# Kernel optimization log

Measured on AMD Instinct MI355X. Metric: run time of the kernel, lower is better.

## Reference

```python
import jax, jax.numpy as jnp
import numpy as np
from jax.ops import segment_sum

N0 = 50000
N1 = 50000
E = 300000
D = 128
L = 3
EPS_GIN = 0.1
COEF = 0.1
BN_EPS = 1e-5


def setup_inputs() -> dict:
    key = jax.random.key(0)
    ks = jax.random.split(key, 32)
    inp = {}
    inp['x0'] = jax.random.randint(ks[0], (N0, 2), 0, 3)
    inp['x1'] = jax.random.randint(ks[1], (N1, 2), 0, 3)
    inp['ei101'] = jax.random.randint(ks[2], (2, E), 0, N1)
    inp['ea101'] = jax.random.randint(ks[3], (E, 2), 0, 3)
    inp['ei110'] = jax.random.randint(ks[4], (2, E), 0, N0)  # src '1' -> dst '0' (N1==N0)
    inp['ea110'] = jax.random.randint(ks[5], (E, 2), 0, 3)
    inp['ei021'] = jax.random.randint(ks[6], (2, E), 0, N1)  # src '0' -> dst '1'
    inp['ea021'] = jax.random.randint(ks[7], (E, 2), 0, 3)
    inp['ei030'] = jax.random.randint(ks[8], (2, E), 0, N0)
    inp['ea030'] = jax.random.randint(ks[9], (E, 2), 0, 3)
    # learned parameters
    s = 0.05
    inp['x_emb1'] = jax.random.normal(ks[10], (120, D), jnp.float32) * s
    inp['x_emb2'] = jax.random.normal(ks[11], (3, D), jnp.float32) * s
    inp['e_emb1'] = jax.random.normal(ks[12], (6, D), jnp.float32) * s
    inp['e_emb2'] = jax.random.normal(ks[13], (3, D), jnp.float32) * s
    w = 1.0 / np.sqrt(D)
    inp['gin_w1'] = jax.random.normal(ks[14], (D, 2 * D), jnp.float32) * w
    inp['gin_b1'] = jnp.zeros((2 * D,), jnp.float32)
    inp['gin_w2'] = jax.random.normal(ks[15], (2 * D, D), jnp.float32) * (1.0 / np.sqrt(2 * D))
    inp['gin_b2'] = jnp.zeros((D,), jnp.float32)
    inp['w110'] = jax.random.normal(ks[16], (D, D), jnp.float32) * w
    inp['b110'] = jnp.zeros((D,), jnp.float32)
    inp['w021'] = jax.random.normal(ks[17], (D, D), jnp.float32) * w
    inp['b021'] = jnp.zeros((D,), jnp.float32)
    inp['w030'] = jax.random.normal(ks[18], (D, D), jnp.float32) * w
    inp['b030'] = jnp.zeros((D,), jnp.float32)
    inp['bn_gamma'] = jnp.ones((L, D), jnp.float32)
    inp['bn_beta'] = jnp.zeros((L, D), jnp.float32)
    return inp


def _add_self_loops(ei, ea, n):
    loop = jnp.arange(n, dtype=ei.dtype)
    ei = jnp.concatenate([ei, jnp.stack([loop, loop])], axis=1)
    self_attr = jnp.tile(jnp.array([[4, 0]], dtype=ea.dtype), (n, 1))
    return ei, jnp.concatenate([ea, self_attr], axis=0)


def _bn(x, gamma, beta):
    # training-mode BatchNorm1d: batch statistics, biased variance
    mu = jnp.mean(x, axis=0)
    var = jnp.var(x, axis=0)
    return (x - mu) * jax.lax.rsqrt(var + BN_EPS) * gamma + beta


def reference(x0, x1, ei101, ea101, ei110, ea110, ei021, ea021, ei030, ea030,
              x_emb1, x_emb2, e_emb1, e_emb2,
              gin_w1, gin_b1, gin_w2, gin_b2,
              w110, b110, w021, b021, w030, b030,
              bn_gamma, bn_beta):
    n0, n1 = x0.shape[0], x1.shape[0]
    # AddSelfLoops only for homogeneous edge types, fill_value=[4,0]
    ei101, ea101 = _add_self_loops(ei101, ea101, n1)
    ei030, ea030 = _add_self_loops(ei030, ea030, n0)

    h0 = x_emb1[x0[:, 0]] + x_emb2[x0[:, 1]]
    h1 = x_emb1[x1[:, 0]] + x_emb2[x1[:, 1]]
    e101 = e_emb1[ea101[:, 0]] + e_emb2[ea101[:, 1]]
    e110 = e_emb1[ea110[:, 0]] + e_emb2[ea110[:, 1]]
    e021 = e_emb1[ea021[:, 0]] + e_emb2[ea021[:, 1]]
    e030 = e_emb1[ea030[:, 0]] + e_emb2[ea030[:, 1]]

    def gin(h_src, h_dst, ei, eattr):
        agg = segment_sum(h_src[ei[0]] + eattr, ei[1], num_segments=h_dst.shape[0])
        z = agg + (1.0 + EPS_GIN) * h_dst
        return jnp.maximum(z @ gin_w1 + gin_b1, 0.0) @ gin_w2 + gin_b2

    def lin(h_src, n_dst, ei, eattr, w, b):
        agg = segment_sum(h_src[ei[0]] + eattr, ei[1], num_segments=n_dst)
        return (agg @ w + b) * COEF

    for layer in range(L):
        # HeteroConv aggr='mean' over convs sharing a destination node type
        out1 = 0.5 * (gin(h1, h1, ei101, e101) + lin(h0, n1, ei021, e021, w021, b021))
        out0 = 0.5 * (lin(h1, n0, ei110, e110, w110, b110) + lin(h0, n0, ei030, e030, w030, b030))
        g, b = bn_gamma[layer], bn_beta[layer]
        h0, h1 = _bn(out0, g, b), _bn(out1, g, b)
        if layer < L - 1:
            h0, h1 = jax.nn.relu(h0), jax.nn.relu(h1)
    # to_homogeneous().x: node types in order '0', '1'
    return jnp.concatenate([h0, h1], axis=0)
```

## Files before the change

### kernel.cpp

```cpp
#include <hip/hip_runtime.h>

#define D 128
#define BN_EPS 1e-5f
#define MAXNB 16

typedef __attribute__((ext_vector_type(8))) short bf16x8;
typedef __attribute__((ext_vector_type(4))) float f32x4;

__device__ __forceinline__ unsigned short f2bf(float x) {
  unsigned u = __float_as_uint(x);
  u += 0x7FFF + ((u >> 16) & 1);
  return (unsigned short)(u >> 16);
}

__device__ __forceinline__ void cvt8(float (&f)[8], bf16x8 r) {
  const unsigned* u = (const unsigned*)&r;
#pragma unroll
  for (int j = 0; j < 4; ++j) {
    f[2 * j] = __uint_as_float(u[j] << 16);
    f[2 * j + 1] = __uint_as_float(u[j] & 0xFFFF0000u);
  }
}

__global__ __launch_bounds__(256) void k_etbl(const float* __restrict__ e1,
                                              const float* __restrict__ e2,
                                              float* __restrict__ etbl) {
  int idx = blockIdx.x * 256 + threadIdx.x;
  if (idx < 9 * D) {
    int combo = idx / D, c = idx % D;
    etbl[idx] = e1[(combo / 3) * D + c] + e2[(combo % 3) * D + c];
  } else if (idx < 10 * D) {
    int c = idx - 9 * D;
    etbl[idx] = e1[4 * D + c] + e2[c];
  }
}

__global__ __launch_bounds__(256) void k_embed(const int* __restrict__ x,
                                               const float* __restrict__ emb1,
                                               const float* __restrict__ emb2,
                                               unsigned short* __restrict__ out,
                                               int n) {
  int idx = blockIdx.x * 256 + threadIdx.x;
  if (idx >= n * 32) return;
  int node = idx >> 5, c4 = idx & 31;
  int i1 = x[2 * node], i2 = x[2 * node + 1];
  float4 v1 = *(const float4*)(emb1 + (size_t)i1 * D + c4 * 4);
  float4 v2 = *(const float4*)(emb2 + (size_t)i2 * D + c4 * 4);
  ushort4 o;
  o.x = f2bf(v1.x + v2.x); o.y = f2bf(v1.y + v2.y);
  o.z = f2bf(v1.z + v2.z); o.w = f2bf(v1.w + v2.w);
  *(ushort4*)(out + (size_t)node * D + c4 * 4) = o;
}

__global__ __launch_bounds__(256) void k_wprep(const float* __restrict__ W,
                                               unsigned short* __restrict__ Wt,
                                               int K, int N, float scale) {
  int idx = blockIdx.x * 256 + threadIdx.x;
  if (idx >= K * N) return;
  int n = idx / K, k = idx - n * K;
  Wt[idx] = f2bf(W[(size_t)k * N + n] * scale);
}

__global__ __launch_bounds__(256) void k_bprep(
    const float* __restrict__ b110, const float* __restrict__ b030,
    const float* __restrict__ gb1, const float* __restrict__ gb2,
    const float* __restrict__ b021, float* __restrict__ bias0,
    float* __restrict__ biash, float* __restrict__ bias1) {
  int i = threadIdx.x;
  if (i < 128) {
    bias0[i] = 0.05f * (b110[i] + b030[i]);
    bias1[i] = 0.5f * gb2[i] + 0.05f * b021[i];
  }
  biash[i] = gb1[i];
}

struct EdgeArr {
  const int* ei[4];
  const int* ea[4];
  int* cur[4];
  int* pay[4];
};
struct CsrPtrs {
  int* cur[4];
  int* rp[4];
  int n[4];
};

__global__ __launch_bounds__(256) void k_hist4(EdgeArr A, int E) {
  int t = blockIdx.y;
  int e = blockIdx.x * 256 + threadIdx.x;
  if (e >= E) return;
  atomicAdd(&A.cur[t][A.ei[t][E + e]], 1);
}

__global__ __launch_bounds__(256) void k_scan1(CsrPtrs p, int* __restrict__ bsum) {
  __shared__ int lds[256];
  int type = blockIdx.y;
  const int* cur = p.cur[type];
  int n = p.n[type];
  int base = blockIdx.x * 4096;
  int s = 0;
  for (int i = threadIdx.x; i < 4096; i += 256) {
    int idx = base + i;
    if (idx < n) s += cur[idx];
  }
  int tid = threadIdx.x;
  lds[tid] = s;
  __syncthreads();
  for (int off = 128; off > 0; off >>= 1) {
    if (tid < off) lds[tid] += lds[tid + off];
    __syncthreads();
  }
  if (tid == 0) bsum[type * MAXNB + blockIdx.x] = lds[0];
}

__global__ __launch_bounds__(64) void k_scan2(int* __restrict__ bsum) {
  int t = threadIdx.x;
  if (t < 4) {
    int run = 0;
    for (int i = 0; i < MAXNB; ++i) {
      int v = bsum[t * MAXNB + i];
      bsum[t * MAXNB + i] = run;
      run += v;
    }
  }
}

__global__ __launch_bounds__(256) void k_scan3(CsrPtrs p,
                                               const int* __restrict__ bsum,
                                               int E) {
  __shared__ int lds[256];
  int type = blockIdx.y;
  int* cur = p.cur[type];
  int* rp = p.rp[type];
  int n = p.n[type];
  int tid = threadIdx.x;
  if (blockIdx.x == 0 && tid == 0) rp[n] = E;
  int t0 = blockIdx.x * 4096 + tid * 16;
  int loc[16];
  int s = 0;
#pragma unroll
  for (int j = 0; j < 16; ++j) {
    int idx = t0 + j;
    int v = (idx < n) ? cur[idx] : 0;
    loc[j] = s;
    s += v;
  }
  lds[tid] = s;
  __syncthreads();
  for (int off = 1; off < 256; off <<= 1) {
    int v = (tid >= off) ? lds[tid - off] : 0;
    __syncthreads();
    lds[tid] += v;
    __syncthreads();
  }
  int off0 = bsum[type * MAXNB + blockIdx.x] + ((tid == 0) ? 0 : lds[tid - 1]);
#pragma unroll
  for (int j = 0; j < 16; ++j) {
    int idx = t0 + j;
    if (idx < n) {
      int v = off0 + loc[j];
      rp[idx] = v;
      cur[idx] = v;
    }
  }
}

__global__ __launch_bounds__(256) void k_fill4(EdgeArr A, int E) {
  int t = blockIdx.y;
  int e = blockIdx.x * 256 + threadIdx.x;
  if (e >= E) return;
  const int* ei = A.ei[t];
  const int* ea = A.ea[t];
  int dst = ei[E + e];
  int src = ei[e];
  int combo = ea[2 * e] * 3 + ea[2 * e + 1];
  int pos = atomicAdd(&A.cur[t][dst], 1);
  A.pay[t][pos] = src | (combo << 16);
}

__global__ __launch_bounds__(256) void k_hnorm(const unsigned short* __restrict__ h,
                                               unsigned short* __restrict__ hn,
                                               const float* __restrict__ bnp,
                                               int n) {
  int idx = blockIdx.x * 256 + threadIdx.x;
  if (idx >= n * 16) return;
  int node = idx >> 4, sl = idx & 15, c = sl * 8;
  bf16x8 v = *(const bf16x8*)(h + (size_t)node * D + c);
  float f[8];
  cvt8(f, v);
  unsigned o[4];
#pragma unroll
  for (int j = 0; j < 4; ++j) {
    float a = fmaxf(fmaf(f[2 * j], bnp[c + 2 * j], bnp[D + c + 2 * j]), 0.f);
    float b = fmaxf(fmaf(f[2 * j + 1], bnp[c + 2 * j + 1], bnp[D + c + 2 * j + 1]), 0.f);
    o[j] = (unsigned)f2bf(a) | ((unsigned)f2bf(b) << 16);
  }
  *(uint4*)(hn + (size_t)node * D + c) = make_uint4(o[0], o[1], o[2], o[3]);
}

struct GArgs {
  const unsigned short* src[4];
  const int* rp[4];
  const int* pay[4];
  unsigned short* agg[4];
  int mode[4];
  int n[4];
};

__device__ __forceinline__ void addet(float (&acc)[8], bf16x8 r,
                                      const float* etp) {
  float f[8];
  cvt8(f, r);
  float4 ea = *(const float4*)etp;
  float4 eb = *(const float4*)(etp + 4);
  acc[0] += f[0] + ea.x; acc[1] += f[1] + ea.y;
  acc[2] += f[2] + ea.z; acc[3] += f[3] + ea.w;
  acc[4] += f[4] + eb.x; acc[5] += f[5] + eb.y;
  acc[6] += f[6] + eb.z; acc[7] += f[7] + eb.w;
}

__global__ __launch_bounds__(256) void k_gather_all(GArgs G,
                                                    const float* __restrict__ etbl) {
  __shared__ float et[10 * D];
  for (int i = threadIdx.x; i < 10 * D; i += 256) et[i] = etbl[i];
  __syncthreads();
  int t = blockIdx.y;
  int n = G.n[t];
  int wv = threadIdx.x >> 6;
  int l = threadIdx.x & 63;
  int grp = l >> 4, sl = l & 15, c = sl * 8;
  const unsigned short* __restrict__ hsrc = G.src[t];
  const int* __restrict__ pay = G.pay[t];
  const int* __restrict__ rp = G.rp[t];
  unsigned short* __restrict__ agg = G.agg[t];
  int mode = G.mode[t];
  int gbase = (blockIdx.x * 4 + wv) * 4;

  for (int i = 0; i < 4; ++i) {
    int g = gbase + i;
    if (g >= n) break;
    float acc[8];
    if (grp == 0 && mode != 0) {
      bf16x8 hv = *(const bf16x8*)(hsrc + (size_t)g * D + c);
      float f[8];
      cvt8(f, hv);
      float m = (mode == 2) ? 2.1f : 1.0f;
#pragma unroll
      for (int j = 0; j < 8; ++j) acc[j] = m * f[j] + et[9 * D + c + j];
    } else {
#pragma unroll
      for (int j = 0; j < 8; ++j) acc[j] = 0.f;
    }
    int e1 = rp[g + 1];
    int e = rp[g] + grp;
    while (e + 4 < e1) {
      int p0 = pay[e];
      int p1 = pay[e + 4];
      bf16x8 r0 = *(const bf16x8*)(hsrc + (size_t)(p0 & 0xFFFF) * D + c);
      bf16x8 r1 = *(const bf16x8*)(hsrc + (size_t)(p1 & 0xFFFF) * D + c);
      addet(acc, r0, et + (p0 >> 16) * D + c);
      addet(acc, r1, et + (p1 >> 16) * D + c);
      e += 8;
    }
    if (e < e1) {
      int p0 = pay[e];
      bf16x8 r0 = *(const bf16x8*)(hsrc + (size_t)(p0 & 0xFFFF) * D + c);
      addet(acc, r0, et + (p0 >> 16) * D + c);
    }
#pragma unroll
    for (int j = 0; j < 8; ++j) {
      acc[j] += __shfl_xor(acc[j], 16);
      acc[j] += __shfl_xor(acc[j], 32);
    }
    if (grp == 0) {
      unsigned o0 = (unsigned)f2bf(acc[0]) | ((unsigned)f2bf(acc[1]) << 16);
      unsigned o1 = (unsigned)f2bf(acc[2]) | ((unsigned)f2bf(acc[3]) << 16);
      unsigned o2 = (unsigned)f2bf(acc[4]) | ((unsigned)f2bf(acc[5]) << 16);
      unsigned o3 = (unsigned)f2bf(acc[6]) | ((unsigned)f2bf(acc[7]) << 16);
      *(uint4*)(agg + (size_t)g * D + c) = make_uint4(o0, o1, o2, o3);
    }
  }
}

template <int NCOLS, int K1, int K2, bool RELU, bool STATS, bool OBF16>
__global__ __launch_bounds__(256) void gemm_breg(
    const unsigned short* __restrict__ A1, const unsigned short* __restrict__ Wt1,
    const unsigned short* __restrict__ A2, const unsigned short* __restrict__ Wt2,
    const float* __restrict__ bias, void* __restrict__ Cv, int M,
    float* __restrict__ stats) {
  constexpr int WC = NCOLS / 4;
  constexpr int CF = WC / 16;
  constexpr int KF1 = K1 / 32;
  constexpr int KF2 = (K2 > 0) ? (K2 / 32) : 1;

  int tid = threadIdx.x;
  int w = tid >> 6, l = tid & 63;
  int lr = l & 15, lk = l >> 4;
  int colbase = w * WC;
  int row0 = blockIdx.x * 64;

  f32x4 acc[4][CF];
#pragma unroll
  for (int rf = 0; rf < 4; ++rf)
#pragma unroll
    for (int cf = 0; cf < CF; ++cf) acc[rf][cf] = (f32x4)(0.f);

  {
    const unsigned short* ap[4];
#pragma unroll
    for (int rf = 0; rf < 4; ++rf) {
      int r = row0 + rf * 16 + lr;
      if (r > M - 1) r = M - 1;
      ap[rf] = A1 + (size_t)r * K1 + lk * 8;
    }
    bf16x8 B[CF][KF1];
#pragma unroll
    for (int cf = 0; cf < CF; ++cf)
#pragma unroll
      for (int kf = 0; kf < KF1; ++kf)
        B[cf][kf] = *(const bf16x8*)(Wt1 + (size_t)(colbase + cf * 16 + lr) * K1 +
                                     kf * 32 + lk * 8);
#pragma unroll
    for (int kf = 0; kf < KF1; ++kf) {
      bf16x8 a[4];
#pragma unroll
      for (int rf = 0; rf < 4; ++rf) a[rf] = *(const bf16x8*)(ap[rf] + kf * 32);
#pragma unroll
      for (int rf = 0; rf < 4; ++rf)
#pragma unroll
        for (int cf = 0; cf < CF; ++cf)
          acc[rf][cf] = __builtin_amdgcn_mfma_f32_16x16x32_bf16(a[rf], B[cf][kf],
                                                                acc[rf][cf], 0, 0, 0);
    }
  }
  if constexpr (K2 > 0) {
    const unsigned short* ap[4];
#pragma unroll
    for (int rf = 0; rf < 4; ++rf) {
      int r = row0 + rf * 16 + lr;
      if (r > M - 1) r = M - 1;
      ap[rf] = A2 + (size_t)r * K2 + lk * 8;
    }
    bf16x8 B[CF][KF2];
#pragma unroll
    for (int cf = 0; cf < CF; ++cf)
#pragma unroll
      for (int kf = 0; kf < KF2; ++kf)
        B[cf][kf] = *(const bf16x8*)(Wt2 + (size_t)(colbase + cf * 16 + lr) * K2 +
                                     kf * 32 + lk * 8);
#pragma unroll
    for (int kf = 0; kf < KF2; ++kf) {
      bf16x8 a[4];
#pragma unroll
      for (int rf = 0; rf < 4; ++rf) a[rf] = *(const bf16x8*)(ap[rf] + kf * 32);
#pragma unroll
      for (int rf = 0; rf < 4; ++rf)
#pragma unroll
        for (int cf = 0; cf < CF; ++cf)
          acc[rf][cf] = __builtin_amdgcn_mfma_f32_16x16x32_bf16(a[rf], B[cf][kf],
                                                                acc[rf][cf], 0, 0, 0);
    }
  }

  float bv[CF];
#pragma unroll
  for (int cf = 0; cf < CF; ++cf) bv[cf] = bias[colbase + cf * 16 + lr];

  float colS[CF], colQ[CF];
#pragma unroll
  for (int cf = 0; cf < CF; ++cf) { colS[cf] = 0.f; colQ[cf] = 0.f; }

  float* Cf = (float*)Cv;
  unsigned short* Cb = (unsigned short*)Cv;
#pragma unroll
  for (int rf = 0; rf < 4; ++rf) {
#pragma unroll
    for (int r = 0; r < 4; ++r) {
      int row = row0 + rf * 16 + lk * 4 + r;
      bool ok = row < M;
#pragma unroll
      for (int cf = 0; cf < CF; ++cf) {
        int col = colbase + cf * 16 + lr;
        float v = acc[rf][cf][r] + bv[cf];
        if (RELU) v = fmaxf(v, 0.f);
        if (ok) {
          if (OBF16)
            Cb[(size_t)row * NCOLS + col] = f2bf(v);
          else
            Cf[(size_t)row * NCOLS + col] = v;
          if (STATS) { colS[cf] += v; colQ[cf] += v * v; }
        }
      }
    }
  }

  if constexpr (STATS) {
#pragma unroll
    for (int cf = 0; cf < CF; ++cf) {
      float s = colS[cf], q = colQ[cf];
      s += __shfl_xor(s, 16); q += __shfl_xor(q, 16);
      s += __shfl_xor(s, 32); q += __shfl_xor(q, 32);
      if (lk == 0) {
        int col = colbase + cf * 16 + lr;
        atomicAdd(&stats[col], s);
        atomicAdd(&stats[D + col], q);
      }
    }
  }
}

__global__ __launch_bounds__(256) void k_bnprep(const float* __restrict__ stats,
                                                const float* __restrict__ gamma,
                                                const float* __restrict__ beta,
                                                float* __restrict__ bnp0,
                                                float* __restrict__ bnp1,
                                                float invM0, float invM1) {
  int i = threadIdx.x;
  if (i < 128) {
    float mu = stats[i] * invM0;
    float var = stats[D + i] * invM0 - mu * mu;
    float sc = rsqrtf(var + BN_EPS) * gamma[i];
    bnp0[i] = sc;
    bnp0[D + i] = beta[i] - mu * sc;
  } else {
    int d = i - 128;
    float mu = stats[2 * D + d] * invM1;
    float var = stats[3 * D + d] * invM1 - mu * mu;
    float sc = rsqrtf(var + BN_EPS) * gamma[d];
    bnp1[d] = sc;
    bnp1[D + d] = beta[d] - mu * sc;
  }
}

__global__ __launch_bounds__(256) void k_bnfin(float* __restrict__ X, int M,
                                               const float* __restrict__ bnp) {
  int idx = blockIdx.x * 256 + threadIdx.x;
  int i = idx >> 5, c4 = idx & 31;
  if (i >= M) return;
  float4 v = *(float4*)(X + (size_t)i * D + c4 * 4);
  float4 sc = *(const float4*)(bnp + c4 * 4);
  float4 sh = *(const float4*)(bnp + D + c4 * 4);
  float4 o;
  o.x = fmaf(v.x, sc.x, sh.x); o.y = fmaf(v.y, sc.y, sh.y);
  o.z = fmaf(v.z, sc.z, sh.z); o.w = fmaf(v.w, sc.w, sh.w);
  *(float4*)(X + (size_t)i * D + c4 * 4) = o;
}

extern "C" void kernel_launch(void* const* d_in, const int* in_sizes, int n_in,
                              void* d_out, int out_size, void* d_ws,
                              size_t ws_size, hipStream_t stream) {
  const int* x0 = (const int*)d_in[0];
  const int* x1 = (const int*)d_in[1];
  const int* ei101 = (const int*)d_in[2];
  const int* ea101 = (const int*)d_in[3];
  const int* ei110 = (const int*)d_in[4];
  const int* ea110 = (const int*)d_in[5];
  const int* ei021 = (const int*)d_in[6];
  const int* ea021 = (const int*)d_in[7];
  const int* ei030 = (const int*)d_in[8];
  const int* ea030 = (const int*)d_in[9];
  const float* x_emb1 = (const float*)d_in[10];
  const float* x_emb2 = (const float*)d_in[11];
  const float* e_emb1 = (const float*)d_in[12];
  const float* e_emb2 = (const float*)d_in[13];
  const float* gin_w1 = (const float*)d_in[14];
  const float* gin_b1 = (const float*)d_in[15];
  const float* gin_w2 = (const float*)d_in[16];
  const float* gin_b2 = (const float*)d_in[17];
  const float* w110 = (const float*)d_in[18];
  const float* b110 = (const float*)d_in[19];
  const float* w021 = (const float*)d_in[20];
  const float* b021 = (const float*)d_in[21];
  const float* w030 = (const float*)d_in[22];
  const float* b030 = (const float*)d_in[23];
  const float* bn_gamma = (const float*)d_in[24];
  const float* bn_beta = (const float*)d_in[25];

  int n0 = in_sizes[0] / 2, n1 = in_sizes[1] / 2;
  int E = in_sizes[2] / 2;
  int nmax = n0 > n1 ? n0 : n1;

  float* h0f = (float*)d_out;
  float* h1f = h0f + (size_t)n0 * D;

  char* p = (char*)d_ws;
  auto alloc = [&](size_t bytes) {
    char* r = p;
    p += (bytes + 63) & ~(size_t)63;
    return r;
  };
  unsigned short* h0r = (unsigned short*)alloc((size_t)n0 * D * 2);
  unsigned short* h1r = (unsigned short*)alloc((size_t)n1 * D * 2);
  unsigned short* hn0 = (unsigned short*)alloc((size_t)n0 * D * 2);
  unsigned short* hn1 = (unsigned short*)alloc((size_t)n1 * D * 2);
  unsigned short* z1b = (unsigned short*)alloc((size_t)n1 * D * 2);
  unsigned short* a021b = (unsigned short*)alloc((size_t)n1 * D * 2);
  unsigned short* a110b = (unsigned short*)alloc((size_t)n0 * D * 2);
  unsigned short* a030b = (unsigned short*)alloc((size_t)n0 * D * 2);
  unsigned short* hiddenb = (unsigned short*)alloc((size_t)n1 * 256 * 2);
  float* etbl = (float*)alloc(10 * D * 4);
  float* stats = (float*)alloc(4 * D * 4);
  float* bnp0 = (float*)alloc(2 * D * 4);
  float* bnp1 = (float*)alloc(2 * D * 4);
  unsigned short* wt110 = (unsigned short*)alloc(128 * 128 * 2);
  unsigned short* wt030 = (unsigned short*)alloc(128 * 128 * 2);
  unsigned short* wt021 = (unsigned short*)alloc(128 * 128 * 2);
  unsigned short* wtg1 = (unsigned short*)alloc(256 * 128 * 2);
  unsigned short* wtg2 = (unsigned short*)alloc(128 * 256 * 2);
  float* bias0 = (float*)alloc(128 * 4);
  float* biash = (float*)alloc(256 * 4);
  float* bias1 = (float*)alloc(128 * 4);

  EdgeArr EA;
  CsrPtrs cp;
  const int* eis[4] = {ei101, ei021, ei110, ei030};
  const int* eas[4] = {ea101, ea021, ea110, ea030};
  int ndst[4] = {n1, n1, n0, n0};
  for (int t = 0; t < 4; ++t) {
    cp.rp[t] = (int*)alloc((size_t)(nmax + 1) * 4);
    cp.cur[t] = (int*)alloc((size_t)nmax * 4);
    EA.pay[t] = (int*)alloc((size_t)E * 4);
    cp.n[t] = ndst[t];
    EA.ei[t] = eis[t];
    EA.ea[t] = eas[t];
    EA.cur[t] = cp.cur[t];
  }
  int* bsum = (int*)alloc(4 * MAXNB * 4);

  dim3 b256(256);
  int eBlocks = (E + 255) / 256;

  k_etbl<<<5, b256, 0, stream>>>(e_emb1, e_emb2, etbl);
  k_embed<<<(n0 * 32 + 255) / 256, b256, 0, stream>>>(x0, x_emb1, x_emb2, h0r, n0);
  k_embed<<<(n1 * 32 + 255) / 256, b256, 0, stream>>>(x1, x_emb1, x_emb2, h1r, n1);
  k_wprep<<<64, b256, 0, stream>>>(w110, wt110, 128, 128, 0.05f);
  k_wprep<<<64, b256, 0, stream>>>(w030, wt030, 128, 128, 0.05f);
  k_wprep<<<64, b256, 0, stream>>>(w021, wt021, 128, 128, 0.05f);
  k_wprep<<<128, b256, 0, stream>>>(gin_w1, wtg1, 128, 256, 1.0f);
  k_wprep<<<128, b256, 0, stream>>>(gin_w2, wtg2, 256, 128, 0.5f);
  k_bprep<<<1, b256, 0, stream>>>(b110, b030, gin_b1, gin_b2, b021, bias0, biash, bias1);

  for (int t = 0; t < 4; ++t)
    hipMemsetAsync(cp.cur[t], 0, (size_t)ndst[t] * sizeof(int), stream);
  k_hist4<<<dim3(eBlocks, 4), b256, 0, stream>>>(EA, E);
  hipMemsetAsync(bsum, 0, 4 * MAXNB * sizeof(int), stream);
  int nb = (nmax + 4095) / 4096;
  k_scan1<<<dim3(nb, 4), b256, 0, stream>>>(cp, bsum);
  k_scan2<<<1, dim3(64), 0, stream>>>(bsum);
  k_scan3<<<dim3(nb, 4), b256, 0, stream>>>(cp, bsum, E);
  k_fill4<<<dim3(eBlocks, 4), b256, 0, stream>>>(EA, E);

  GArgs GA;
  GA.agg[0] = z1b;   GA.mode[0] = 2; GA.n[0] = n1;
  GA.agg[1] = a021b; GA.mode[1] = 0; GA.n[1] = n1;
  GA.agg[2] = a110b; GA.mode[2] = 0; GA.n[2] = n0;
  GA.agg[3] = a030b; GA.mode[3] = 1; GA.n[3] = n0;
  for (int t = 0; t < 4; ++t) {
    GA.rp[t] = cp.rp[t];
    GA.pay[t] = EA.pay[t];
  }

  int mB0 = (n0 + 63) / 64, mB1 = (n1 + 63) / 64;
  dim3 gGrid((nmax + 15) / 16, 4);

  for (int layer = 0; layer < 3; ++layer) {
    const unsigned short* s0 = (layer == 0) ? h0r : hn0;
    const unsigned short* s1 = (layer == 0) ? h1r : hn1;
    GA.src[0] = s1; GA.src[1] = s0; GA.src[2] = s1; GA.src[3] = s0;
    k_gather_all<<<gGrid, b256, 0, stream>>>(GA, etbl);

    hipMemsetAsync(stats, 0, 4 * D * sizeof(float), stream);

    if (layer < 2) {
      gemm_breg<128, 128, 128, false, true, true><<<mB0, b256, 0, stream>>>(
          a110b, wt110, a030b, wt030, bias0, h0r, n0, stats);
      gemm_breg<256, 128, 0, true, false, true><<<mB1, b256, 0, stream>>>(
          z1b, wtg1, nullptr, nullptr, biash, hiddenb, n1, nullptr);
      gemm_breg<128, 256, 128, false, true, true><<<mB1, b256, 0, stream>>>(
          hiddenb, wtg2, a021b, wt021, bias1, h1r, n1, stats + 2 * D);
    } else {
      gemm_breg<128, 128, 128, false, true, false><<<mB0, b256, 0, stream>>>(
          a110b, wt110, a030b, wt030, bias0, h0f, n0, stats);
      gemm_breg<256, 128, 0, true, false, true><<<mB1, b256, 0, stream>>>(
          z1b, wtg1, nullptr, nullptr, biash, hiddenb, n1, nullptr);
      gemm_breg<128, 256, 128, false, true, false><<<mB1, b256, 0, stream>>>(
          hiddenb, wtg2, a021b, wt021, bias1, h1f, n1, stats + 2 * D);
    }

    k_bnprep<<<1, b256, 0, stream>>>(stats, bn_gamma + layer * D,
                                     bn_beta + layer * D, bnp0, bnp1,
                                     1.0f / n0, 1.0f / n1);
    if (layer < 2) {
      k_hnorm<<<(n0 * 16 + 255) / 256, b256, 0, stream>>>(h0r, hn0, bnp0, n0);
      k_hnorm<<<(n1 * 16 + 255) / 256, b256, 0, stream>>>(h1r, hn1, bnp1, n1);
    } else {
      k_bnfin<<<(n0 * 32 + 255) / 256, b256, 0, stream>>>(h0f, n0, bnp0);
      k_bnfin<<<(n1 * 32 + 255) / 256, b256, 0, stream>>>(h1f, n1, bnp1);
    }
  }
}
```

Baseline: 799.2 us.

## Precompute per-node edge-embedding sums once and partition CSR build by destination range

The edge-attribute embedding sum plus self-loop term for each destination node does not change across layers, so it is now computed once into a bf16 base buffer per edge type. Each layer's gather then loads that base row instead of adding an embedding-table row for every edge. The CSR histogram and fill kernels are also split into 8 destination ranges per edge chunk, so atomics land on a smaller address range at the cost of reading the edge list eight times. The change costs extra memory and traffic for the base buffers, and the base is rounded to bf16 before accumulation.

```diff
diff --git a/kernel.cpp b/kernel.cpp
--- a/kernel.cpp
+++ b/kernel.cpp
@@ -74,6 +74,7 @@
   biash[i] = gb1[i];
 }
 
+#define ECHUNK 2048
 struct EdgeArr {
   const int* ei[4];
   const int* ea[4];
@@ -86,11 +87,19 @@
   int n[4];
 };
 
-__global__ __launch_bounds__(256) void k_hist4(EdgeArr A, int E) {
+__global__ __launch_bounds__(256) void k_hist_part(EdgeArr A, int E, int rsz) {
   int t = blockIdx.y;
-  int e = blockIdx.x * 256 + threadIdx.x;
-  if (e >= E) return;
-  atomicAdd(&A.cur[t][A.ei[t][E + e]], 1);
+  int r = blockIdx.x & 7;
+  int chunk = blockIdx.x >> 3;
+  const int* dstp = A.ei[t] + E;
+  int* cur = A.cur[t];
+  int lo = r * rsz, hi = lo + rsz;
+  int base = chunk * ECHUNK;
+  int end = min(base + ECHUNK, E);
+  for (int e = base + (int)threadIdx.x; e < end; e += 256) {
+    int dst = dstp[e];
+    if (dst >= lo && dst < hi) atomicAdd(&cur[dst], 1);
+  }
 }
 
 __global__ __launch_bounds__(256) void k_scan1(CsrPtrs p, int* __restrict__ bsum) {
@@ -166,17 +175,155 @@
   }
 }
 
-__global__ __launch_bounds__(256) void k_fill4(EdgeArr A, int E) {
+__global__ __launch_bounds__(256) void k_fill_part(EdgeArr A, int E, int rsz) {
   int t = blockIdx.y;
-  int e = blockIdx.x * 256 + threadIdx.x;
-  if (e >= E) return;
+  int r = blockIdx.x & 7;
+  int chunk = blockIdx.x >> 3;
   const int* ei = A.ei[t];
   const int* ea = A.ea[t];
-  int dst = ei[E + e];
-  int src = ei[e];
-  int combo = ea[2 * e] * 3 + ea[2 * e + 1];
-  int pos = atomicAdd(&A.cur[t][dst], 1);
-  A.pay[t][pos] = src | (combo << 16);
+  int* cur = A.cur[t];
+  int* pay = A.pay[t];
+  int lo = r * rsz, hi = lo + rsz;
+  int base = chunk * ECHUNK;
+  int end = min(base + ECHUNK, E);
+  for (int e = base + (int)threadIdx.x; e < end; e += 256) {
+    int dst = ei[E + e];
+    if (dst >= lo && dst < hi) {
+      int src = ei[e];
+      int combo = ea[2 * e] * 3 + ea[2 * e + 1];
+      int pos = atomicAdd(&cur[dst], 1);
+      pay[pos] = src | (combo << 16);
+    }
+  }
+}
+
+struct GArgs {
+  const unsigned short* src[4];
+  const unsigned short* base[4];
+  const int* rp[4];
+  const int* pay[4];
+  unsigned short* agg[4];
+  int mode[4];
+  int n[4];
+};
+
+__global__ __launch_bounds__(256) void k_base(GArgs G,
+                                              const float* __restrict__ etbl) {
+  __shared__ float et[10 * D];
+  for (int i = threadIdx.x; i < 10 * D; i += 256) et[i] = etbl[i];
+  __syncthreads();
+  int t = blockIdx.y;
+  int n = G.n[t];
+  int wv = threadIdx.x >> 6;
+  int l = threadIdx.x & 63;
+  int grp = l >> 4, sl = l & 15, c = sl * 8;
+  const int* __restrict__ pay = G.pay[t];
+  const int* __restrict__ rp = G.rp[t];
+  unsigned short* __restrict__ outb = (unsigned short*)G.base[t];
+  int mode = G.mode[t];
+  int gbase = (blockIdx.x * 4 + wv) * 4;
+
+  for (int i = 0; i < 4; ++i) {
+    int g = gbase + i;
+    if (g >= n) break;
+    float acc[8];
+    if (grp == 0 && mode != 0) {
+#pragma unroll
+      for (int j = 0; j < 8; ++j) acc[j] = et[9 * D + c + j];
+    } else {
+#pragma unroll
+      for (int j = 0; j < 8; ++j) acc[j] = 0.f;
+    }
+    int e1 = rp[g + 1];
+    for (int e = rp[g] + grp; e < e1; e += 4) {
+      int combo = pay[e] >> 16;
+      const float* etp = et + combo * D + c;
+#pragma unroll
+      for (int j = 0; j < 8; ++j) acc[j] += etp[j];
+    }
+#pragma unroll
+    for (int j = 0; j < 8; ++j) {
+      acc[j] += __shfl_xor(acc[j], 16);
+      acc[j] += __shfl_xor(acc[j], 32);
+    }
+    if (grp == 0) {
+      unsigned o0 = (unsigned)f2bf(acc[0]) | ((unsigned)f2bf(acc[1]) << 16);
+      unsigned o1 = (unsigned)f2bf(acc[2]) | ((unsigned)f2bf(acc[3]) << 16);
+      unsigned o2 = (unsigned)f2bf(acc[4]) | ((unsigned)f2bf(acc[5]) << 16);
+      unsigned o3 = (unsigned)f2bf(acc[6]) | ((unsigned)f2bf(acc[7]) << 16);
+      *(uint4*)(outb + (size_t)g * D + c) = make_uint4(o0, o1, o2, o3);
+    }
+  }
+}
+
+__global__ __launch_bounds__(256) void k_gather_all(GArgs G) {
+  int t = blockIdx.y;
+  int n = G.n[t];
+  int wv = threadIdx.x >> 6;
+  int l = threadIdx.x & 63;
+  int grp = l >> 4, sl = l & 15, c = sl * 8;
+  const unsigned short* __restrict__ hsrc = G.src[t];
+  const unsigned short* __restrict__ baseb = G.base[t];
+  const int* __restrict__ pay = G.pay[t];
+  const int* __restrict__ rp = G.rp[t];
+  unsigned short* __restrict__ agg = G.agg[t];
+  int mode = G.mode[t];
+  int gbase = (blockIdx.x * 4 + wv) * 4;
+
+  for (int i = 0; i < 4; ++i) {
+    int g = gbase + i;
+    if (g >= n) break;
+    float acc[8];
+    if (grp == 0) {
+      bf16x8 bv = *(const bf16x8*)(baseb + (size_t)g * D + c);
+      cvt8(acc, bv);
+      if (mode != 0) {
+        bf16x8 hv = *(const bf16x8*)(hsrc + (size_t)g * D + c);
+        float f[8];
+        cvt8(f, hv);
+        float m = (mode == 2) ? 2.1f : 1.0f;
+#pragma unroll
+        for (int j = 0; j < 8; ++j) acc[j] += m * f[j];
+      }
+    } else {
+#pragma unroll
+      for (int j = 0; j < 8; ++j) acc[j] = 0.f;
+    }
+    int e1 = rp[g + 1];
+    int e = rp[g] + grp;
+    while (e + 4 < e1) {
+      int p0 = pay[e] & 0xFFFF;
+      int p1 = pay[e + 4] & 0xFFFF;
+      bf16x8 r0 = *(const bf16x8*)(hsrc + (size_t)p0 * D + c);
+      bf16x8 r1 = *(const bf16x8*)(hsrc + (size_t)p1 * D + c);
+      float f0[8], f1[8];
+      cvt8(f0, r0);
+      cvt8(f1, r1);
+#pragma unroll
+      for (int j = 0; j < 8; ++j) acc[j] += f0[j] + f1[j];
+      e += 8;
+    }
+    if (e < e1) {
+      int p0 = pay[e] & 0xFFFF;
+      bf16x8 r0 = *(const bf16x8*)(hsrc + (size_t)p0 * D + c);
+      float f0[8];
+      cvt8(f0, r0);
+#pragma unroll
+      for (int j = 0; j < 8; ++j) acc[j] += f0[j];
+    }
+#pragma unroll
+    for (int j = 0; j < 8; ++j) {
+      acc[j] += __shfl_xor(acc[j], 16);
+      acc[j] += __shfl_xor(acc[j], 32);
+    }
+    if (grp == 0) {
+      unsigned o0 = (unsigned)f2bf(acc[0]) | ((unsigned)f2bf(acc[1]) << 16);
+      unsigned o1 = (unsigned)f2bf(acc[2]) | ((unsigned)f2bf(acc[3]) << 16);
+      unsigned o2 = (unsigned)f2bf(acc[4]) | ((unsigned)f2bf(acc[5]) << 16);
+      unsigned o3 = (unsigned)f2bf(acc[6]) | ((unsigned)f2bf(acc[7]) << 16);
+      *(uint4*)(agg + (size_t)g * D + c) = make_uint4(o0, o1, o2, o3);
+    }
+  }
 }
 
 __global__ __launch_bounds__(256) void k_hnorm(const unsigned short* __restrict__ h,
@@ -197,90 +344,6 @@
     o[j] = (unsigned)f2bf(a) | ((unsigned)f2bf(b) << 16);
   }
   *(uint4*)(hn + (size_t)node * D + c) = make_uint4(o[0], o[1], o[2], o[3]);
-}
-
-struct GArgs {
-  const unsigned short* src[4];
-  const int* rp[4];
-  const int* pay[4];
-  unsigned short* agg[4];
-  int mode[4];
-  int n[4];
-};
-
-__device__ __forceinline__ void addet(float (&acc)[8], bf16x8 r,
-                                      const float* etp) {
-  float f[8];
-  cvt8(f, r);
-  float4 ea = *(const float4*)etp;
-  float4 eb = *(const float4*)(etp + 4);
-  acc[0] += f[0] + ea.x; acc[1] += f[1] + ea.y;
-  acc[2] += f[2] + ea.z; acc[3] += f[3] + ea.w;
-  acc[4] += f[4] + eb.x; acc[5] += f[5] + eb.y;
-  acc[6] += f[6] + eb.z; acc[7] += f[7] + eb.w;
-}
-
-__global__ __launch_bounds__(256) void k_gather_all(GArgs G,
-                                                    const float* __restrict__ etbl) {
-  __shared__ float et[10 * D];
-  for (int i = threadIdx.x; i < 10 * D; i += 256) et[i] = etbl[i];
-  __syncthreads();
-  int t = blockIdx.y;
-  int n = G.n[t];
-  int wv = threadIdx.x >> 6;
-  int l = threadIdx.x & 63;
-  int grp = l >> 4, sl = l & 15, c = sl * 8;
-  const unsigned short* __restrict__ hsrc = G.src[t];
-  const int* __restrict__ pay = G.pay[t];
-  const int* __restrict__ rp = G.rp[t];
-  unsigned short* __restrict__ agg = G.agg[t];
-  int mode = G.mode[t];
-  int gbase = (blockIdx.x * 4 + wv) * 4;
-
-  for (int i = 0; i < 4; ++i) {
-    int g = gbase + i;
-    if (g >= n) break;
-    float acc[8];
-    if (grp == 0 && mode != 0) {
-      bf16x8 hv = *(const bf16x8*)(hsrc + (size_t)g * D + c);
-      float f[8];
-      cvt8(f, hv);
-      float m = (mode == 2) ? 2.1f : 1.0f;
-#pragma unroll
-      for (int j = 0; j < 8; ++j) acc[j] = m * f[j] + et[9 * D + c + j];
-    } else {
-#pragma unroll
-      for (int j = 0; j < 8; ++j) acc[j] = 0.f;
-    }
-    int e1 = rp[g + 1];
-    int e = rp[g] + grp;
-    while (e + 4 < e1) {
-      int p0 = pay[e];
-      int p1 = pay[e + 4];
-      bf16x8 r0 = *(const bf16x8*)(hsrc + (size_t)(p0 & 0xFFFF) * D + c);
-      bf16x8 r1 = *(const bf16x8*)(hsrc + (size_t)(p1 & 0xFFFF) * D + c);
-      addet(acc, r0, et + (p0 >> 16) * D + c);
-      addet(acc, r1, et + (p1 >> 16) * D + c);
-      e += 8;
-    }
-    if (e < e1) {
-      int p0 = pay[e];
-      bf16x8 r0 = *(const bf16x8*)(hsrc + (size_t)(p0 & 0xFFFF) * D + c);
-      addet(acc, r0, et + (p0 >> 16) * D + c);
-    }
-#pragma unroll
-    for (int j = 0; j < 8; ++j) {
-      acc[j] += __shfl_xor(acc[j], 16);
-      acc[j] += __shfl_xor(acc[j], 32);
-    }
-    if (grp == 0) {
-      unsigned o0 = (unsigned)f2bf(acc[0]) | ((unsigned)f2bf(acc[1]) << 16);
-      unsigned o1 = (unsigned)f2bf(acc[2]) | ((unsigned)f2bf(acc[3]) << 16);
-      unsigned o2 = (unsigned)f2bf(acc[4]) | ((unsigned)f2bf(acc[5]) << 16);
-      unsigned o3 = (unsigned)f2bf(acc[6]) | ((unsigned)f2bf(acc[7]) << 16);
-      *(uint4*)(agg + (size_t)g * D + c) = make_uint4(o0, o1, o2, o3);
-    }
-  }
 }
 
 template <int NCOLS, int K1, int K2, bool RELU, bool STATS, bool OBF16>
@@ -499,6 +562,9 @@
   unsigned short* a110b = (unsigned short*)alloc((size_t)n0 * D * 2);
   unsigned short* a030b = (unsigned short*)alloc((size_t)n0 * D * 2);
   unsigned short* hiddenb = (unsigned short*)alloc((size_t)n1 * 256 * 2);
+  unsigned short* baseb[4];
+  for (int t = 0; t < 4; ++t)
+    baseb[t] = (unsigned short*)alloc((size_t)nmax * D * 2);
   float* etbl = (float*)alloc(10 * D * 4);
   float* stats = (float*)alloc(4 * D * 4);
   float* bnp0 = (float*)alloc(2 * D * 4);
@@ -529,7 +595,6 @@
   int* bsum = (int*)alloc(4 * MAXNB * 4);
 
   dim3 b256(256);
-  int eBlocks = (E + 255) / 256;
 
   k_etbl<<<5, b256, 0, stream>>>(e_emb1, e_emb2, etbl);
   k_embed<<<(n0 * 32 + 255) / 256, b256, 0, stream>>>(x0, x_emb1, x_emb2, h0r, n0);
@@ -543,13 +608,16 @@
 
   for (int t = 0; t < 4; ++t)
     hipMemsetAsync(cp.cur[t], 0, (size_t)ndst[t] * sizeof(int), stream);
-  k_hist4<<<dim3(eBlocks, 4), b256, 0, stream>>>(EA, E);
+  int rsz = (nmax + 7) / 8;
+  int nchunks = (E + ECHUNK - 1) / ECHUNK;
+  dim3 partGrid(nchunks * 8, 4);
+  k_hist_part<<<partGrid, b256, 0, stream>>>(EA, E, rsz);
   hipMemsetAsync(bsum, 0, 4 * MAXNB * sizeof(int), stream);
   int nb = (nmax + 4095) / 4096;
   k_scan1<<<dim3(nb, 4), b256, 0, stream>>>(cp, bsum);
   k_scan2<<<1, dim3(64), 0, stream>>>(bsum);
   k_scan3<<<dim3(nb, 4), b256, 0, stream>>>(cp, bsum, E);
-  k_fill4<<<dim3(eBlocks, 4), b256, 0, stream>>>(EA, E);
+  k_fill_part<<<partGrid, b256, 0, stream>>>(EA, E, rsz);
 
   GArgs GA;
   GA.agg[0] = z1b;   GA.mode[0] = 2; GA.n[0] = n1;
@@ -559,16 +627,19 @@
   for (int t = 0; t < 4; ++t) {
     GA.rp[t] = cp.rp[t];
     GA.pay[t] = EA.pay[t];
-  }
+    GA.base[t] = baseb[t];
+  }
+
+  dim3 gGrid((nmax + 15) / 16, 4);
+  k_base<<<gGrid, b256, 0, stream>>>(GA, etbl);
 
   int mB0 = (n0 + 63) / 64, mB1 = (n1 + 63) / 64;
-  dim3 gGrid((nmax + 15) / 16, 4);
 
   for (int layer = 0; layer < 3; ++layer) {
     const unsigned short* s0 = (layer == 0) ? h0r : hn0;
     const unsigned short* s1 = (layer == 0) ? h1r : hn1;
     GA.src[0] = s1; GA.src[1] = s0; GA.src[2] = s1; GA.src[3] = s0;
-    k_gather_all<<<gGrid, b256, 0, stream>>>(GA, etbl);
+    k_gather_all<<<gGrid, b256, 0, stream>>>(GA);
 
     hipMemsetAsync(stats, 0, 4 * D * sizeof(float), stream);
 
```

Measured after the change: 836.0 us. +4.6%, slower.

## Fuse neighbor gather into GEMM kernels and range-partition CSR build atomics

Applied to the files above, without the earlier changes.

Removes the standalone gather kernel. Each fused GEMM block now aggregates neighbor features for its 64 rows straight into a swizzled LDS tile and feeds MFMA from there, so the bf16 aggregate buffers no longer make a round trip through global memory. The histogram and fill kernels are split into 8 destination-range partitions per edge chunk, to localize atomics and improve cache locality, at the cost of reading each edge 8 times. Ping-pong output buffers are added so the gather source is not overwritten while still being read, and the edge-table LDS rows are padded. The risk is lower GEMM occupancy from the serial gather inside each block and extra LDS use.

```diff
diff --git a/kernel.cpp b/kernel.cpp
--- a/kernel.cpp
+++ b/kernel.cpp
@@ -74,6 +74,7 @@
   biash[i] = gb1[i];
 }
 
+#define ECHUNK 2048
 struct EdgeArr {
   const int* ei[4];
   const int* ea[4];
@@ -86,11 +87,19 @@
   int n[4];
 };
 
-__global__ __launch_bounds__(256) void k_hist4(EdgeArr A, int E) {
+__global__ __launch_bounds__(256) void k_hist_part(EdgeArr A, int E, int rsz) {
   int t = blockIdx.y;
-  int e = blockIdx.x * 256 + threadIdx.x;
-  if (e >= E) return;
-  atomicAdd(&A.cur[t][A.ei[t][E + e]], 1);
+  int r = blockIdx.x & 7;
+  int chunk = blockIdx.x >> 3;
+  const int* dstp = A.ei[t] + E;
+  int* cur = A.cur[t];
+  int lo = r * rsz, hi = lo + rsz;
+  int base = chunk * ECHUNK;
+  int end = min(base + ECHUNK, E);
+  for (int e = base + (int)threadIdx.x; e < end; e += 256) {
+    int dst = dstp[e];
+    if (dst >= lo && dst < hi) atomicAdd(&cur[dst], 1);
+  }
 }
 
 __global__ __launch_bounds__(256) void k_scan1(CsrPtrs p, int* __restrict__ bsum) {
@@ -166,17 +175,26 @@
   }
 }
 
-__global__ __launch_bounds__(256) void k_fill4(EdgeArr A, int E) {
+__global__ __launch_bounds__(256) void k_fill_part(EdgeArr A, int E, int rsz) {
   int t = blockIdx.y;
-  int e = blockIdx.x * 256 + threadIdx.x;
-  if (e >= E) return;
+  int r = blockIdx.x & 7;
+  int chunk = blockIdx.x >> 3;
   const int* ei = A.ei[t];
   const int* ea = A.ea[t];
-  int dst = ei[E + e];
-  int src = ei[e];
-  int combo = ea[2 * e] * 3 + ea[2 * e + 1];
-  int pos = atomicAdd(&A.cur[t][dst], 1);
-  A.pay[t][pos] = src | (combo << 16);
+  int* cur = A.cur[t];
+  int* pay = A.pay[t];
+  int lo = r * rsz, hi = lo + rsz;
+  int base = chunk * ECHUNK;
+  int end = min(base + ECHUNK, E);
+  for (int e = base + (int)threadIdx.x; e < end; e += 256) {
+    int dst = ei[E + e];
+    if (dst >= lo && dst < hi) {
+      int src = ei[e];
+      int combo = ea[2 * e] * 3 + ea[2 * e + 1];
+      int pos = atomicAdd(&cur[dst], 1);
+      pay[pos] = src | (combo << 16);
+    }
+  }
 }
 
 __global__ __launch_bounds__(256) void k_hnorm(const unsigned short* __restrict__ h,
@@ -199,55 +217,47 @@
   *(uint4*)(hn + (size_t)node * D + c) = make_uint4(o[0], o[1], o[2], o[3]);
 }
 
-struct GArgs {
-  const unsigned short* src[4];
-  const int* rp[4];
-  const int* pay[4];
-  unsigned short* agg[4];
-  int mode[4];
-  int n[4];
+constexpr int ETLD = 132;
+
+struct FArgs {
+  const unsigned short* a1;
+  const unsigned short* hs1;
+  const int* rp1;
+  const int* pay1;
+  int mode1;
+  const unsigned short* wt1;
+  const unsigned short* hs2;
+  const int* rp2;
+  const int* pay2;
+  int mode2;
+  const unsigned short* wt2;
+  const float* etbl;
+  const float* bias;
+  void* c;
+  float* stats;
+  int M;
 };
 
-__device__ __forceinline__ void addet(float (&acc)[8], bf16x8 r,
-                                      const float* etp) {
-  float f[8];
-  cvt8(f, r);
-  float4 ea = *(const float4*)etp;
-  float4 eb = *(const float4*)(etp + 4);
-  acc[0] += f[0] + ea.x; acc[1] += f[1] + ea.y;
-  acc[2] += f[2] + ea.z; acc[3] += f[3] + ea.w;
-  acc[4] += f[4] + eb.x; acc[5] += f[5] + eb.y;
-  acc[6] += f[6] + eb.z; acc[7] += f[7] + eb.w;
-}
-
-__global__ __launch_bounds__(256) void k_gather_all(GArgs G,
-                                                    const float* __restrict__ etbl) {
-  __shared__ float et[10 * D];
-  for (int i = threadIdx.x; i < 10 * D; i += 256) et[i] = etbl[i];
-  __syncthreads();
-  int t = blockIdx.y;
-  int n = G.n[t];
-  int wv = threadIdx.x >> 6;
-  int l = threadIdx.x & 63;
-  int grp = l >> 4, sl = l & 15, c = sl * 8;
-  const unsigned short* __restrict__ hsrc = G.src[t];
-  const int* __restrict__ pay = G.pay[t];
-  const int* __restrict__ rp = G.rp[t];
-  unsigned short* __restrict__ agg = G.agg[t];
-  int mode = G.mode[t];
-  int gbase = (blockIdx.x * 4 + wv) * 4;
-
-  for (int i = 0; i < 4; ++i) {
-    int g = gbase + i;
-    if (g >= n) break;
+__device__ __forceinline__ void gather_tile(
+    unsigned short* At, const unsigned short* __restrict__ hsrc,
+    const int* __restrict__ rp, const int* __restrict__ pay, int mode,
+    const float* et, int row0, int M, int w, int grp, int sl, int c) {
+  for (int i = 0; i < 16; ++i) {
+    int r = w * 16 + i;
+    int g = row0 + r;
+    if (g >= M) break;
     float acc[8];
     if (grp == 0 && mode != 0) {
       bf16x8 hv = *(const bf16x8*)(hsrc + (size_t)g * D + c);
       float f[8];
       cvt8(f, hv);
       float m = (mode == 2) ? 2.1f : 1.0f;
-#pragma unroll
-      for (int j = 0; j < 8; ++j) acc[j] = m * f[j] + et[9 * D + c + j];
+      float4 ea = *(const float4*)(et + 9 * ETLD + c);
+      float4 eb = *(const float4*)(et + 9 * ETLD + c + 4);
+      acc[0] = m * f[0] + ea.x; acc[1] = m * f[1] + ea.y;
+      acc[2] = m * f[2] + ea.z; acc[3] = m * f[3] + ea.w;
+      acc[4] = m * f[4] + eb.x; acc[5] = m * f[5] + eb.y;
+      acc[6] = m * f[6] + eb.z; acc[7] = m * f[7] + eb.w;
     } else {
 #pragma unroll
       for (int j = 0; j < 8; ++j) acc[j] = 0.f;
@@ -255,18 +265,37 @@
     int e1 = rp[g + 1];
     int e = rp[g] + grp;
     while (e + 4 < e1) {
-      int p0 = pay[e];
-      int p1 = pay[e + 4];
+      int p0 = pay[e], p1 = pay[e + 4];
       bf16x8 r0 = *(const bf16x8*)(hsrc + (size_t)(p0 & 0xFFFF) * D + c);
       bf16x8 r1 = *(const bf16x8*)(hsrc + (size_t)(p1 & 0xFFFF) * D + c);
-      addet(acc, r0, et + (p0 >> 16) * D + c);
-      addet(acc, r1, et + (p1 >> 16) * D + c);
+      const float* t0 = et + (p0 >> 16) * ETLD + c;
+      const float* t1 = et + (p1 >> 16) * ETLD + c;
+      float f0[8], f1[8];
+      cvt8(f0, r0);
+      cvt8(f1, r1);
+      float4 a0 = *(const float4*)t0, b0 = *(const float4*)(t0 + 4);
+      float4 a1v = *(const float4*)t1, b1v = *(const float4*)(t1 + 4);
+      acc[0] += (f0[0] + a0.x) + (f1[0] + a1v.x);
+      acc[1] += (f0[1] + a0.y) + (f1[1] + a1v.y);
+      acc[2] += (f0[2] + a0.z) + (f1[2] + a1v.z);
+      acc[3] += (f0[3] + a0.w) + (f1[3] + a1v.w);
+      acc[4] += (f0[4] + b0.x) + (f1[4] + b1v.x);
+      acc[5] += (f0[5] + b0.y) + (f1[5] + b1v.y);
+      acc[6] += (f0[6] + b0.z) + (f1[6] + b1v.z);
+      acc[7] += (f0[7] + b0.w) + (f1[7] + b1v.w);
       e += 8;
     }
     if (e < e1) {
       int p0 = pay[e];
       bf16x8 r0 = *(const bf16x8*)(hsrc + (size_t)(p0 & 0xFFFF) * D + c);
-      addet(acc, r0, et + (p0 >> 16) * D + c);
+      const float* t0 = et + (p0 >> 16) * ETLD + c;
+      float f0[8];
+      cvt8(f0, r0);
+      float4 a0 = *(const float4*)t0, b0 = *(const float4*)(t0 + 4);
+      acc[0] += f0[0] + a0.x; acc[1] += f0[1] + a0.y;
+      acc[2] += f0[2] + a0.z; acc[3] += f0[3] + a0.w;
+      acc[4] += f0[4] + b0.x; acc[5] += f0[5] + b0.y;
+      acc[6] += f0[6] + b0.z; acc[7] += f0[7] + b0.w;
     }
 #pragma unroll
     for (int j = 0; j < 8; ++j) {
@@ -278,28 +307,41 @@
       unsigned o1 = (unsigned)f2bf(acc[2]) | ((unsigned)f2bf(acc[3]) << 16);
       unsigned o2 = (unsigned)f2bf(acc[4]) | ((unsigned)f2bf(acc[5]) << 16);
       unsigned o3 = (unsigned)f2bf(acc[6]) | ((unsigned)f2bf(acc[7]) << 16);
-      *(uint4*)(agg + (size_t)g * D + c) = make_uint4(o0, o1, o2, o3);
-    }
-  }
-}
-
-template <int NCOLS, int K1, int K2, bool RELU, bool STATS, bool OBF16>
-__global__ __launch_bounds__(256) void gemm_breg(
-    const unsigned short* __restrict__ A1, const unsigned short* __restrict__ Wt1,
-    const unsigned short* __restrict__ A2, const unsigned short* __restrict__ Wt2,
-    const float* __restrict__ bias, void* __restrict__ Cv, int M,
-    float* __restrict__ stats) {
+      *(uint4*)(At + r * 128 + ((sl * 8) ^ ((r & 7) << 3))) =
+          make_uint4(o0, o1, o2, o3);
+    }
+  }
+}
+
+template <int NCOLS, int K1, int K2, bool G1, bool G2, bool RELU, bool STATS,
+          bool OBF16>
+__global__ __launch_bounds__(256) void k_fused(FArgs F) {
   constexpr int WC = NCOLS / 4;
   constexpr int CF = WC / 16;
   constexpr int KF1 = K1 / 32;
-  constexpr int KF2 = (K2 > 0) ? (K2 / 32) : 1;
+  constexpr int KF2 = (K2 > 0) ? K2 / 32 : 1;
+  static_assert(!G1 || K1 == 128, "gathered source must be K=128");
+  static_assert(K2 == 0 || G2, "source 2 must be gathered when present");
+  __shared__ float et[10 * ETLD];
+  __shared__ unsigned short At1[G1 ? 64 * 128 : 8];
+  __shared__ unsigned short At2[G2 ? 64 * 128 : 8];
 
   int tid = threadIdx.x;
   int w = tid >> 6, l = tid & 63;
+  int grp = l >> 4, sl = l & 15, c = sl * 8;
   int lr = l & 15, lk = l >> 4;
+  int row0 = blockIdx.x * 64;
+  int M = F.M;
+
+  for (int i = tid; i < 10 * D; i += 256)
+    et[(i >> 7) * ETLD + (i & 127)] = F.etbl[i];
+  __syncthreads();
+
+  if (G1) gather_tile(At1, F.hs1, F.rp1, F.pay1, F.mode1, et, row0, M, w, grp, sl, c);
+  if (G2) gather_tile(At2, F.hs2, F.rp2, F.pay2, F.mode2, et, row0, M, w, grp, sl, c);
+  __syncthreads();
+
   int colbase = w * WC;
-  int row0 = blockIdx.x * 64;
-
   f32x4 acc[4][CF];
 #pragma unroll
   for (int rf = 0; rf < 4; ++rf)
@@ -308,24 +350,33 @@
 
   {
     const unsigned short* ap[4];
-#pragma unroll
-    for (int rf = 0; rf < 4; ++rf) {
-      int r = row0 + rf * 16 + lr;
-      if (r > M - 1) r = M - 1;
-      ap[rf] = A1 + (size_t)r * K1 + lk * 8;
+    if (!G1) {
+#pragma unroll
+      for (int rf = 0; rf < 4; ++rf) {
+        int r = row0 + rf * 16 + lr;
+        if (r > M - 1) r = M - 1;
+        ap[rf] = F.a1 + (size_t)r * K1 + lk * 8;
+      }
     }
     bf16x8 B[CF][KF1];
 #pragma unroll
     for (int cf = 0; cf < CF; ++cf)
 #pragma unroll
       for (int kf = 0; kf < KF1; ++kf)
-        B[cf][kf] = *(const bf16x8*)(Wt1 + (size_t)(colbase + cf * 16 + lr) * K1 +
+        B[cf][kf] = *(const bf16x8*)(F.wt1 + (size_t)(colbase + cf * 16 + lr) * K1 +
                                      kf * 32 + lk * 8);
 #pragma unroll
     for (int kf = 0; kf < KF1; ++kf) {
       bf16x8 a[4];
-#pragma unroll
-      for (int rf = 0; rf < 4; ++rf) a[rf] = *(const bf16x8*)(ap[rf] + kf * 32);
+      if (G1) {
+#pragma unroll
+        for (int rf = 0; rf < 4; ++rf)
+          a[rf] = *(const bf16x8*)(At1 + (rf * 16 + lr) * 128 +
+                                   ((kf * 32 + lk * 8) ^ ((lr & 7) << 3)));
+      } else {
+#pragma unroll
+        for (int rf = 0; rf < 4; ++rf) a[rf] = *(const bf16x8*)(ap[rf] + kf * 32);
+      }
 #pragma unroll
       for (int rf = 0; rf < 4; ++rf)
 #pragma unroll
@@ -335,25 +386,20 @@
     }
   }
   if constexpr (K2 > 0) {
-    const unsigned short* ap[4];
-#pragma unroll
-    for (int rf = 0; rf < 4; ++rf) {
-      int r = row0 + rf * 16 + lr;
-      if (r > M - 1) r = M - 1;
-      ap[rf] = A2 + (size_t)r * K2 + lk * 8;
-    }
     bf16x8 B[CF][KF2];
 #pragma unroll
     for (int cf = 0; cf < CF; ++cf)
 #pragma unroll
       for (int kf = 0; kf < KF2; ++kf)
-        B[cf][kf] = *(const bf16x8*)(Wt2 + (size_t)(colbase + cf * 16 + lr) * K2 +
+        B[cf][kf] = *(const bf16x8*)(F.wt2 + (size_t)(colbase + cf * 16 + lr) * K2 +
                                      kf * 32 + lk * 8);
 #pragma unroll
     for (int kf = 0; kf < KF2; ++kf) {
       bf16x8 a[4];
 #pragma unroll
-      for (int rf = 0; rf < 4; ++rf) a[rf] = *(const bf16x8*)(ap[rf] + kf * 32);
+      for (int rf = 0; rf < 4; ++rf)
+        a[rf] = *(const bf16x8*)(At2 + (rf * 16 + lr) * 128 +
+                                 ((kf * 32 + lk * 8) ^ ((lr & 7) << 3)));
 #pragma unroll
       for (int rf = 0; rf < 4; ++rf)
 #pragma unroll
@@ -365,14 +411,14 @@
 
   float bv[CF];
 #pragma unroll
-  for (int cf = 0; cf < CF; ++cf) bv[cf] = bias[colbase + cf * 16 + lr];
+  for (int cf = 0; cf < CF; ++cf) bv[cf] = F.bias[colbase + cf * 16 + lr];
 
   float colS[CF], colQ[CF];
 #pragma unroll
   for (int cf = 0; cf < CF; ++cf) { colS[cf] = 0.f; colQ[cf] = 0.f; }
 
-  float* Cf = (float*)Cv;
-  unsigned short* Cb = (unsigned short*)Cv;
+  float* Cf = (float*)F.c;
+  unsigned short* Cb = (unsigned short*)F.c;
 #pragma unroll
   for (int rf = 0; rf < 4; ++rf) {
 #pragma unroll
@@ -403,8 +449,8 @@
       s += __shfl_xor(s, 32); q += __shfl_xor(q, 32);
       if (lk == 0) {
         int col = colbase + cf * 16 + lr;
-        atomicAdd(&stats[col], s);
-        atomicAdd(&stats[D + col], q);
+        atomicAdd(&F.stats[col], s);
+        atomicAdd(&F.stats[D + col], q);
       }
     }
   }
@@ -492,12 +538,10 @@
   };
   unsigned short* h0r = (unsigned short*)alloc((size_t)n0 * D * 2);
   unsigned short* h1r = (unsigned short*)alloc((size_t)n1 * D * 2);
+  unsigned short* h0o = (unsigned short*)alloc((size_t)n0 * D * 2);
+  unsigned short* h1o = (unsigned short*)alloc((size_t)n1 * D * 2);
   unsigned short* hn0 = (unsigned short*)alloc((size_t)n0 * D * 2);
   unsigned short* hn1 = (unsigned short*)alloc((size_t)n1 * D * 2);
-  unsigned short* z1b = (unsigned short*)alloc((size_t)n1 * D * 2);
-  unsigned short* a021b = (unsigned short*)alloc((size_t)n1 * D * 2);
-  unsigned short* a110b = (unsigned short*)alloc((size_t)n0 * D * 2);
-  unsigned short* a030b = (unsigned short*)alloc((size_t)n0 * D * 2);
   unsigned short* hiddenb = (unsigned short*)alloc((size_t)n1 * 256 * 2);
   float* etbl = (float*)alloc(10 * D * 4);
   float* stats = (float*)alloc(4 * D * 4);
@@ -529,7 +573,6 @@
   int* bsum = (int*)alloc(4 * MAXNB * 4);
 
   dim3 b256(256);
-  int eBlocks = (E + 255) / 256;
 
   k_etbl<<<5, b256, 0, stream>>>(e_emb1, e_emb2, etbl);
   k_embed<<<(n0 * 32 + 255) / 256, b256, 0, stream>>>(x0, x_emb1, x_emb2, h0r, n0);
@@ -543,57 +586,67 @@
 
   for (int t = 0; t < 4; ++t)
     hipMemsetAsync(cp.cur[t], 0, (size_t)ndst[t] * sizeof(int), stream);
-  k_hist4<<<dim3(eBlocks, 4), b256, 0, stream>>>(EA, E);
+  int rsz = (nmax + 7) / 8;
+  int nchunks = (E + ECHUNK - 1) / ECHUNK;
+  dim3 partGrid(nchunks * 8, 4);
+  k_hist_part<<<partGrid, b256, 0, stream>>>(EA, E, rsz);
   hipMemsetAsync(bsum, 0, 4 * MAXNB * sizeof(int), stream);
   int nb = (nmax + 4095) / 4096;
   k_scan1<<<dim3(nb, 4), b256, 0, stream>>>(cp, bsum);
   k_scan2<<<1, dim3(64), 0, stream>>>(bsum);
   k_scan3<<<dim3(nb, 4), b256, 0, stream>>>(cp, bsum, E);
-  k_fill4<<<dim3(eBlocks, 4), b256, 0, stream>>>(EA, E);
-
-  GArgs GA;
-  GA.agg[0] = z1b;   GA.mode[0] = 2; GA.n[0] = n1;
-  GA.agg[1] = a021b; GA.mode[1] = 0; GA.n[1] = n1;
-  GA.agg[2] = a110b; GA.mode[2] = 0; GA.n[2] = n0;
-  GA.agg[3] = a030b; GA.mode[3] = 1; GA.n[3] = n0;
-  for (int t = 0; t < 4; ++t) {
-    GA.rp[t] = cp.rp[t];
-    GA.pay[t] = EA.pay[t];
-  }
+  k_fill_part<<<partGrid, b256, 0, stream>>>(EA, E, rsz);
 
   int mB0 = (n0 + 63) / 64, mB1 = (n1 + 63) / 64;
-  dim3 gGrid((nmax + 15) / 16, 4);
 
   for (int layer = 0; layer < 3; ++layer) {
     const unsigned short* s0 = (layer == 0) ? h0r : hn0;
     const unsigned short* s1 = (layer == 0) ? h1r : hn1;
-    GA.src[0] = s1; GA.src[1] = s0; GA.src[2] = s1; GA.src[3] = s0;
-    k_gather_all<<<gGrid, b256, 0, stream>>>(GA, etbl);
 
     hipMemsetAsync(stats, 0, 4 * D * sizeof(float), stream);
 
+    FArgs Fh = {};
+    Fh.hs1 = s1; Fh.rp1 = cp.rp[0]; Fh.pay1 = EA.pay[0]; Fh.mode1 = 2;
+    Fh.wt1 = wtg1;
+    Fh.etbl = etbl; Fh.bias = biash; Fh.c = hiddenb; Fh.stats = nullptr;
+    Fh.M = n1;
+    k_fused<256, 128, 0, true, false, true, false, true>
+        <<<mB1, b256, 0, stream>>>(Fh);
+
+    FArgs F0 = {};
+    F0.hs1 = s1; F0.rp1 = cp.rp[2]; F0.pay1 = EA.pay[2]; F0.mode1 = 0;
+    F0.wt1 = wt110;
+    F0.hs2 = s0; F0.rp2 = cp.rp[3]; F0.pay2 = EA.pay[3]; F0.mode2 = 1;
+    F0.wt2 = wt030;
+    F0.etbl = etbl; F0.bias = bias0; F0.stats = stats; F0.M = n0;
+    FArgs F1 = {};
+    F1.a1 = hiddenb; F1.wt1 = wtg2;
+    F1.hs2 = s0; F1.rp2 = cp.rp[1]; F1.pay2 = EA.pay[1]; F1.mode2 = 0;
+    F1.wt2 = wt021;
+    F1.etbl = etbl; F1.bias = bias1; F1.stats = stats + 2 * D; F1.M = n1;
+
     if (layer < 2) {
-      gemm_breg<128, 128, 128, false, true, true><<<mB0, b256, 0, stream>>>(
-          a110b, wt110, a030b, wt030, bias0, h0r, n0, stats);
-      gemm_breg<256, 128, 0, true, false, true><<<mB1, b256, 0, stream>>>(
-          z1b, wtg1, nullptr, nullptr, biash, hiddenb, n1, nullptr);
-      gemm_breg<128, 256, 128, false, true, true><<<mB1, b256, 0, stream>>>(
-          hiddenb, wtg2, a021b, wt021, bias1, h1r, n1, stats + 2 * D);
+      F0.c = h0o;
+      k_fused<128, 128, 128, true, true, false, true, true>
+          <<<mB0, b256, 0, stream>>>(F0);
+      F1.c = h1o;
+      k_fused<128, 256, 128, false, true, false, true, true>
+          <<<mB1, b256, 0, stream>>>(F1);
     } else {
-      gemm_breg<128, 128, 128, false, true, false><<<mB0, b256, 0, stream>>>(
-          a110b, wt110, a030b, wt030, bias0, h0f, n0, stats);
-      gemm_breg<256, 128, 0, true, false, true><<<mB1, b256, 0, stream>>>(
-          z1b, wtg1, nullptr, nullptr, biash, hiddenb, n1, nullptr);
-      gemm_breg<128, 256, 128, false, true, false><<<mB1, b256, 0, stream>>>(
-          hiddenb, wtg2, a021b, wt021, bias1, h1f, n1, stats + 2 * D);
+      F0.c = h0f;
+      k_fused<128, 128, 128, true, true, false, true, false>
+          <<<mB0, b256, 0, stream>>>(F0);
+      F1.c = h1f;
+      k_fused<128, 256, 128, false, true, false, true, false>
+          <<<mB1, b256, 0, stream>>>(F1);
     }
 
     k_bnprep<<<1, b256, 0, stream>>>(stats, bn_gamma + layer * D,
                                      bn_beta + layer * D, bnp0, bnp1,
                                      1.0f / n0, 1.0f / n1);
     if (layer < 2) {
-      k_hnorm<<<(n0 * 16 + 255) / 256, b256, 0, stream>>>(h0r, hn0, bnp0, n0);
-      k_hnorm<<<(n1 * 16 + 255) / 256, b256, 0, stream>>>(h1r, hn1, bnp1, n1);
+      k_hnorm<<<(n0 * 16 + 255) / 256, b256, 0, stream>>>(h0o, hn0, bnp0, n0);
+      k_hnorm<<<(n1 * 16 + 255) / 256, b256, 0, stream>>>(h1o, hn1, bnp1, n1);
     } else {
       k_bnfin<<<(n0 * 32 + 255) / 256, b256, 0, stream>>>(h0f, n0, bnp0);
       k_bnfin<<<(n1 * 32 + 255) / 256, b256, 0, stream>>>(h1f, n1, bnp1);
```

Result: slower. 918.6 us (+14.9%).
